# Optimization experiments

Measured on AMD Instinct MI355X. Metric: run time of the kernel, lower is better.

Reference implementation:

```python
import jax, jax.numpy as jnp
import numpy as np

N_HARMONIC = 8
FRAME_SHIFT = 240
SR = 24000
ALPHA = 0.1
SIGMA = 0.003
B = 32
N_FRAMES = 500


def setup_inputs() -> dict:
    key = jax.random.key(0)
    k1, k2, k3, k4 = jax.random.split(key, 4)
    u = jax.random.uniform(k1, (B, N_FRAMES), dtype=jnp.float32)
    f0s = jnp.where(u < 0.1, 0.0, 80.0 + u * 320.0)
    # random phase per harmonic in [-pi, 0], phi[0] = 0 (matches torch init)
    phi = jax.random.uniform(k2, (N_HARMONIC,), dtype=jnp.float32) * (-np.pi)
    phi = phi.at[0].set(0.0)
    amplitude = jax.random.normal(k3, (N_HARMONIC + 1,), dtype=jnp.float32)
    # per-harmonic gaussian noise N(0, sigma) at sample rate
    noise = SIGMA * jax.random.normal(
        k4, (N_HARMONIC, B, N_FRAMES * FRAME_SHIFT), dtype=jnp.float32)
    return {"f0s": f0s, "phi": phi, "amplitude": amplitude, "noise": noise}


def reference(f0s, phi, amplitude, noise):
    # upsample frame-rate f0 to sample rate: [B, n_frames] -> [B, T]
    f0_up = jnp.repeat(f0s, FRAME_SHIFT, axis=1)
    # cumsum is linear in harmonic index: compute once, scale by (i+1)
    cs = jnp.cumsum(2.0 * np.pi * f0_up / SR, axis=1)            # [B, T]
    k = jnp.arange(1, N_HARMONIC + 1, dtype=f0s.dtype)           # [H]
    sin_all = jnp.sin(k[:, None, None] * cs[None] + phi[:, None, None])  # [H, B, T]
    pos = (f0_up > 0).astype(f0s.dtype)                          # [B, T]
    zero = (f0_up == 0).astype(f0s.dtype)                        # [B, T]
    # excitation per harmonic: voiced -> alpha*sin + noise; unvoiced -> scaled noise
    exc = (ALPHA * sin_all + noise) * pos + zero * (ALPHA / (3.0 * SIGMA)) * noise
    out = jnp.tanh(jnp.einsum('h,hbt->bt', amplitude[:N_HARMONIC], exc)
                   + amplitude[N_HARMONIC])
    return out
```

## Files before the change

### kernel.cpp

```cpp
#include <hip/hip_runtime.h>
#include <math.h>

constexpr int   BB   = 32;
constexpr int   NF   = 500;
constexpr int   FS   = 240;
constexpr int   TT   = NF * FS;
constexpr int   HH   = 8;
constexpr float ALPHA = 0.1f;

__global__ __launch_bounds__(64) void frame_scan(const float* __restrict__ f0s,
                                                 float2* __restrict__ ws2) {
    const int b    = blockIdx.x;
    const int lane = threadIdx.x;

    const float  TWO_PI_F = 6.28318530717958647692f;
    const double INV_2PI  = 0.15915494309189533576;

    double d[8];
    double sum = 0.0;
#pragma unroll
    for (int i = 0; i < 8; ++i) {
        const int f = lane * 8 + i;
        const float f0   = (f < NF) ? f0s[b * NF + f] : 0.0f;
        const float dphi = (TWO_PI_F * f0) / 24000.0f;
        d[i] = (double)dphi * INV_2PI;
        sum += d[i];
    }

    const double mine = sum * 240.0;
    double run = mine;
    for (int delta = 1; delta < 64; delta <<= 1) {
        const double o = __shfl_up(run, delta, 64);
        if (lane >= delta) run += o;
    }
    double acc = run - mine;

#pragma unroll
    for (int i = 0; i < 8; ++i) {
        const int f = lane * 8 + i;
        if (f < NF) {
            const double fr = acc - rint(acc);
            ws2[b * NF + f] = make_float2((float)fr, (float)d[i]);
        }
        acc += d[i] * 240.0;
    }
}

__device__ __forceinline__ float sin_rev(float fr) {
#if __has_builtin(__builtin_amdgcn_sinf)
    return __builtin_amdgcn_sinf(fr);
#else
    return __sinf(fr * 6.28318530717958647692f);
#endif
}

__global__ __launch_bounds__(256) void synth(const float* __restrict__ phi,
                                             const float* __restrict__ amp,
                                             const float* __restrict__ noise,
                                             const float2* __restrict__ ws2,
                                             float* __restrict__ out) {
    const int g  = blockIdx.x * 256 + threadIdx.x;
    const int s4 = g * 4;
    const int b  = s4 / TT;
    const int t  = s4 - b * TT;
    const int f  = t / FS;
    const int j  = t - f * FS;

    const float2 fd = ws2[b * NF + f];
    const float  dr = fd.y;
    const bool   voiced = (dr > 0.0f);

    float cs[4];
    cs[0] = fd.x + (float)(j + 1) * dr;
    cs[1] = cs[0] + dr;
    cs[2] = cs[1] + dr;
    cs[3] = cs[2] + dr;

    const float INV2PIf = 0.15915494309189533576f;

    float sdot[4] = {0.f, 0.f, 0.f, 0.f};
    float ndot[4] = {0.f, 0.f, 0.f, 0.f};
    float kcs[4]  = {0.f, 0.f, 0.f, 0.f};

#pragma unroll
    for (int h = 0; h < HH; ++h) {
        const float a  = amp[h];
        const float ph = phi[h] * INV2PIf;
        const float4 nh = *reinterpret_cast<const float4*>(
            noise + ((size_t)(h * BB + b) * TT + t));

        ndot[0] = fmaf(a, nh.x, ndot[0]);
        ndot[1] = fmaf(a, nh.y, ndot[1]);
        ndot[2] = fmaf(a, nh.z, ndot[2]);
        ndot[3] = fmaf(a, nh.w, ndot[3]);

#pragma unroll
        for (int e = 0; e < 4; ++e) {
            kcs[e] += cs[e];
            const float r  = kcs[e] + ph;
            const float fr = r - rintf(r);
            sdot[e] = fmaf(a, sin_rev(fr), sdot[e]);
        }
    }

    const float a8 = amp[HH];
    const float UV = (float)(0.1 / (3.0 * 0.003));

    float4 o;
    float* op = reinterpret_cast<float*>(&o);
#pragma unroll
    for (int e = 0; e < 4; ++e) {
        const float x = voiced ? fmaf(ALPHA, sdot[e], ndot[e]) : UV * ndot[e];
        op[e] = tanhf(x + a8);
    }
    *reinterpret_cast<float4*>(out + (size_t)b * TT + t) = o;
}

extern "C" void kernel_launch(void* const* d_in, const int* in_sizes, int n_in,
                              void* d_out, int out_size, void* d_ws, size_t ws_size,
                              hipStream_t stream) {
    const float* f0s   = (const float*)d_in[0];
    const float* phi   = (const float*)d_in[1];
    const float* amp   = (const float*)d_in[2];
    const float* noise = (const float*)d_in[3];
    float* out = (float*)d_out;
    float2* ws2 = (float2*)d_ws;

    frame_scan<<<BB, 64, 0, stream>>>(f0s, ws2);

    const int nthreads = BB * TT / 4;
    synth<<<nthreads / 256, 256, 0, stream>>>(phi, amp, noise, ws2, out);
}
```

Measured before the change: 32.72 us.

## Fuse frame scan into synth kernel with per-block redundant scan in LDS

Drops the separate frame_scan launch. Each synth block now recomputes the full 500-frame phase prefix scan for its batch row in shared memory, using one wavefront, before synthesizing samples. Each thread also handles 8 samples instead of 4, and the grid becomes 2D (time blocks × batch). This removes one kernel launch and the workspace round trip, but every block repeats the double-precision scan and the other waves sit idle at the barrier until it finishes.

Result: faster. 30.10 us (-8.0%).

```diff
diff --git a/kernel.cpp b/kernel.cpp
--- a/kernel.cpp
+++ b/kernel.cpp
@@ -1,50 +1,15 @@
 #include <hip/hip_runtime.h>
 #include <math.h>
 
-constexpr int   BB   = 32;
-constexpr int   NF   = 500;
-constexpr int   FS   = 240;
-constexpr int   TT   = NF * FS;
-constexpr int   HH   = 8;
+constexpr int   BB    = 32;
+constexpr int   NF    = 500;
+constexpr int   FS    = 240;
+constexpr int   TT    = NF * FS;
+constexpr int   HH    = 8;
 constexpr float ALPHA = 0.1f;
 
-__global__ __launch_bounds__(64) void frame_scan(const float* __restrict__ f0s,
-                                                 float2* __restrict__ ws2) {
-    const int b    = blockIdx.x;
-    const int lane = threadIdx.x;
-
-    const float  TWO_PI_F = 6.28318530717958647692f;
-    const double INV_2PI  = 0.15915494309189533576;
-
-    double d[8];
-    double sum = 0.0;
-#pragma unroll
-    for (int i = 0; i < 8; ++i) {
-        const int f = lane * 8 + i;
-        const float f0   = (f < NF) ? f0s[b * NF + f] : 0.0f;
-        const float dphi = (TWO_PI_F * f0) / 24000.0f;
-        d[i] = (double)dphi * INV_2PI;
-        sum += d[i];
-    }
-
-    const double mine = sum * 240.0;
-    double run = mine;
-    for (int delta = 1; delta < 64; delta <<= 1) {
-        const double o = __shfl_up(run, delta, 64);
-        if (lane >= delta) run += o;
-    }
-    double acc = run - mine;
-
-#pragma unroll
-    for (int i = 0; i < 8; ++i) {
-        const int f = lane * 8 + i;
-        if (f < NF) {
-            const double fr = acc - rint(acc);
-            ws2[b * NF + f] = make_float2((float)fr, (float)d[i]);
-        }
-        acc += d[i] * 240.0;
-    }
-}
+constexpr int SPT = 8;
+constexpr int BLK = 256;
 
 __device__ __forceinline__ float sin_rev(float fr) {
 #if __has_builtin(__builtin_amdgcn_sinf)
@@ -54,48 +19,95 @@
 #endif
 }
 
-__global__ __launch_bounds__(256) void synth(const float* __restrict__ phi,
-                                             const float* __restrict__ amp,
-                                             const float* __restrict__ noise,
-                                             const float2* __restrict__ ws2,
-                                             float* __restrict__ out) {
-    const int g  = blockIdx.x * 256 + threadIdx.x;
-    const int s4 = g * 4;
-    const int b  = s4 / TT;
-    const int t  = s4 - b * TT;
-    const int f  = t / FS;
-    const int j  = t - f * FS;
+__global__ __launch_bounds__(BLK) void synth_fused(const float* __restrict__ f0s,
+                                                   const float* __restrict__ phi,
+                                                   const float* __restrict__ amp,
+                                                   const float* __restrict__ noise,
+                                                   float* __restrict__ out) {
+    const int b   = blockIdx.y;
+    const int tid = threadIdx.x;
 
-    const float2 fd = ws2[b * NF + f];
+    __shared__ float2 sfr[NF];
+
+    if (tid < 64) {
+        const int lane = tid;
+        const float  TWO_PI_F = 6.28318530717958647692f;
+        const double INV_2PI  = 0.15915494309189533576;
+
+        double d[8];
+        double sum = 0.0;
+#pragma unroll
+        for (int i = 0; i < 8; ++i) {
+            const int f = lane * 8 + i;
+            const float f0   = (f < NF) ? f0s[b * NF + f] : 0.0f;
+            const float dphi = (TWO_PI_F * f0) / 24000.0f;
+            d[i] = (double)dphi * INV_2PI;
+            sum += d[i];
+        }
+
+        const double mine = sum * 240.0;
+        double run = mine;
+        for (int delta = 1; delta < 64; delta <<= 1) {
+            const double o = __shfl_up(run, delta, 64);
+            if (lane >= delta) run += o;
+        }
+        double acc = run - mine;
+
+#pragma unroll
+        for (int i = 0; i < 8; ++i) {
+            const int f = lane * 8 + i;
+            if (f < NF) {
+                const double fr = acc - rint(acc);
+                sfr[f] = make_float2((float)fr, (float)d[i]);
+            }
+            acc += d[i] * 240.0;
+        }
+    }
+    __syncthreads();
+
+    const int t = (blockIdx.x * BLK + tid) * SPT;
+    if (t >= TT) return;
+
+    const int f = t / FS;
+    const int j = t - f * FS;
+
+    const float2 fd = sfr[f];
     const float  dr = fd.y;
     const bool   voiced = (dr > 0.0f);
 
-    float cs[4];
+    float cs[SPT];
     cs[0] = fd.x + (float)(j + 1) * dr;
-    cs[1] = cs[0] + dr;
-    cs[2] = cs[1] + dr;
-    cs[3] = cs[2] + dr;
+#pragma unroll
+    for (int e = 1; e < SPT; ++e) cs[e] = cs[e - 1] + dr;
 
     const float INV2PIf = 0.15915494309189533576f;
 
-    float sdot[4] = {0.f, 0.f, 0.f, 0.f};
-    float ndot[4] = {0.f, 0.f, 0.f, 0.f};
-    float kcs[4]  = {0.f, 0.f, 0.f, 0.f};
+    float sdot[SPT], ndot[SPT], kcs[SPT];
+#pragma unroll
+    for (int e = 0; e < SPT; ++e) { sdot[e] = 0.f; ndot[e] = 0.f; kcs[e] = 0.f; }
+
+    const size_t base = (size_t)b * TT + t;
 
 #pragma unroll
     for (int h = 0; h < HH; ++h) {
         const float a  = amp[h];
         const float ph = phi[h] * INV2PIf;
-        const float4 nh = *reinterpret_cast<const float4*>(
-            noise + ((size_t)(h * BB + b) * TT + t));
+        const float4* np4 = reinterpret_cast<const float4*>(
+            noise + (size_t)h * (BB * (size_t)TT) + base);
+        const float4 n0 = np4[0];
+        const float4 n1 = np4[1];
 
-        ndot[0] = fmaf(a, nh.x, ndot[0]);
-        ndot[1] = fmaf(a, nh.y, ndot[1]);
-        ndot[2] = fmaf(a, nh.z, ndot[2]);
-        ndot[3] = fmaf(a, nh.w, ndot[3]);
+        ndot[0] = fmaf(a, n0.x, ndot[0]);
+        ndot[1] = fmaf(a, n0.y, ndot[1]);
+        ndot[2] = fmaf(a, n0.z, ndot[2]);
+        ndot[3] = fmaf(a, n0.w, ndot[3]);
+        ndot[4] = fmaf(a, n1.x, ndot[4]);
+        ndot[5] = fmaf(a, n1.y, ndot[5]);
+        ndot[6] = fmaf(a, n1.z, ndot[6]);
+        ndot[7] = fmaf(a, n1.w, ndot[7]);
 
 #pragma unroll
-        for (int e = 0; e < 4; ++e) {
+        for (int e = 0; e < SPT; ++e) {
             kcs[e] += cs[e];
             const float r  = kcs[e] + ph;
             const float fr = r - rintf(r);
@@ -106,14 +118,20 @@
     const float a8 = amp[HH];
     const float UV = (float)(0.1 / (3.0 * 0.003));
 
-    float4 o;
-    float* op = reinterpret_cast<float*>(&o);
+    float4 o0, o1;
+    float* op = reinterpret_cast<float*>(&o0);
+    float tmp[SPT];
 #pragma unroll
-    for (int e = 0; e < 4; ++e) {
+    for (int e = 0; e < SPT; ++e) {
         const float x = voiced ? fmaf(ALPHA, sdot[e], ndot[e]) : UV * ndot[e];
-        op[e] = tanhf(x + a8);
+        tmp[e] = tanhf(x + a8);
     }
-    *reinterpret_cast<float4*>(out + (size_t)b * TT + t) = o;
+    o0 = make_float4(tmp[0], tmp[1], tmp[2], tmp[3]);
+    o1 = make_float4(tmp[4], tmp[5], tmp[6], tmp[7]);
+    float4* ov = reinterpret_cast<float4*>(out + base);
+    ov[0] = o0;
+    ov[1] = o1;
+    (void)op;
 }
 
 extern "C" void kernel_launch(void* const* d_in, const int* in_sizes, int n_in,
@@ -124,10 +142,8 @@
     const float* amp   = (const float*)d_in[2];
     const float* noise = (const float*)d_in[3];
     float* out = (float*)d_out;
-    float2* ws2 = (float2*)d_ws;
 
-    frame_scan<<<BB, 64, 0, stream>>>(f0s, ws2);
-
-    const int nthreads = BB * TT / 4;
-    synth<<<nthreads / 256, 256, 0, stream>>>(phi, amp, noise, ws2, out);
+    const int blocks_x = (TT / SPT + BLK - 1) / BLK;
+    dim3 grid(blocks_x, BB);
+    synth_fused<<<grid, BLK, 0, stream>>>(f0s, phi, amp, noise, out);
 }
```
